# Optimization experiments

Measured on AMD Instinct MI355X. Metric: run time of the kernel, lower is better.

## Reference

```python
import jax, jax.numpy as jnp
import numpy as np

BETA = 0.25

def setup_inputs() -> dict:
    key = jax.random.key(0)
    k1, k2 = jax.random.split(key)
    z_e = jax.random.normal(k1, (32, 256, 32, 32), dtype=jnp.float32)
    embed_weight = jax.random.normal(k2, (4096, 256), dtype=jnp.float32) * 0.1
    return {"z_e": z_e, "embed_weight": embed_weight}

def reference(z_e, embed_weight):
    # Eval-mode forward (no input noise, no EMA buffer update).
    B, C, H, W = z_e.shape
    K = embed_weight.shape[0]
    z_t = jnp.transpose(z_e, (0, 2, 3, 1))            # [B,H,W,C]
    z_flat = z_t.reshape(-1, C)                        # [N,C]
    # Squared Euclidean distances; argmin is identical to argmin of cdist(p=2).
    d = (
        jnp.sum(z_flat * z_flat, axis=1, keepdims=True)
        - 2.0 * (z_flat @ embed_weight.T)
        + jnp.sum(embed_weight * embed_weight, axis=1)
    )                                                  # [N,K]
    idx = jnp.argmin(d, axis=1)                        # [N]
    # utilization = (#unique codes used) / vocab_size, jit-safe via bincount-style scatter
    counts = jnp.zeros((K,), dtype=jnp.float32).at[idx].add(1.0)
    utilization = jnp.sum(counts > 0).astype(jnp.float32) / K
    z_q = embed_weight[idx].reshape(B, H, W, C)        # [B,H,W,C]
    commitment_loss = jnp.mean((jax.lax.stop_gradient(z_q) - z_t) ** 2) * BETA
    z_q_st = z_t + jax.lax.stop_gradient(z_q - z_t)    # straight-through
    return jnp.transpose(z_q_st, (0, 3, 1, 2)), commitment_loss, utilization
```

## Files before the change

### kernel.cpp

```cpp
#include <hip/hip_runtime.h>
#include <math.h>


#define WGAP 52

using half8 = __attribute__((ext_vector_type(8))) _Float16;
using f32x4 = __attribute__((ext_vector_type(4))) float;

__device__ __forceinline__ void gload_lds16(const void* g, void* l) {
  __builtin_amdgcn_global_load_lds(
      (const __attribute__((address_space(1))) unsigned int*)g,
      (__attribute__((address_space(3))) unsigned int*)l, 16, 0, 0);
}

__device__ __forceinline__ bool lexlt64(double v, int x, double ov, int ox) {
  return (v < ov) || (v == ov && x < ox);
}

__device__ __forceinline__ int med3i(int a, int b, int c) {
  int d;
  asm("v_med3_i32 %0, %1, %2, %3" : "=v"(d) : "v"(a), "v"(b), "v"(c));
  return d;
}

__device__ __forceinline__ void ins3k(int key, int& a0, int& a1, int& a2) {
  const int n2 = min(a2, max(key, a1));
  const int n1 = med3i(key, a0, a1);
  a0 = min(key, a0);
  a1 = n1;
  a2 = n2;
}

__device__ __forceinline__ void mrg3k(int& a0, int& a1, int& a2,
                                      int b0, int b1, int b2) {
  const int c0 = min(a0, b0);
  const int x = max(a0, b0);
  const int y = min(a1, b1);
  const int c1 = min(x, y);
  const int z = max(x, y);
  const int ww = min(a2, b2);
  const int c2 = min(z, ww);
  a0 = c0; a1 = c1; a2 = c2;
}

__global__ __launch_bounds__(256) void vq_prep(const float* __restrict__ E,
                                               uint4* __restrict__ Epk,
                                               float* __restrict__ en1024,
                                               int* __restrict__ used,
                                               double* __restrict__ lossSum,
                                               int* __restrict__ candCount,
                                               int* __restrict__ messyCount) {
  const int t = blockIdx.x * 256 + threadIdx.x;
  if (t < 4096) used[t] = 0;
  if (t == 4096) *lossSum = 0.0;
  if (t == 4097) *candCount = 0;
  if (t == 4098) *messyCount = 0;
  const int code = t >> 5, j = t & 31;
  const int rc = code & 63;
  const int khalf = j >> 4, jo = j & 15;
  const float* src = E + (size_t)code * 256 + j * 8;
  const float4 v0 = *(const float4*)(src);
  const float4 v1 = *(const float4*)(src + 4);
  float zv[8] = {v0.x, v0.y, v0.z, v0.w, v1.x, v1.y, v1.z, v1.w};
  union { half8 h; uint4 u; } pk;
  float s = 0.f;
#pragma unroll
  for (int e = 0; e < 8; ++e) {
    const float z = zv[e];
    s = fmaf(z, z, s);
    pk.h[e] = (_Float16)(z * 256.0f);
  }
  const size_t g = (size_t)((code >> 6) * 2 + khalf) * 1024 +
                   rc * 16 + (jo ^ (rc & 15));
  Epk[g] = pk.u;
#pragma unroll
  for (int off = 1; off < 32; off <<= 1) s += __shfl_xor(s, off);
  if (j == 0) en1024[code] = s * 1024.0f;
}

__global__ __launch_bounds__(256, 3) void vq_screen(
    const float* __restrict__ Z, const char* __restrict__ Epk,
    const float* __restrict__ en1024,
    int* __restrict__ pk0, int* __restrict__ pk1, int* __restrict__ pk2) {
  __shared__ char lds[32768];
  const int tid = threadIdx.x;
  const int w = tid >> 6, l = tid & 63;
  const int xcd = blockIdx.x & 7, inner = blockIdx.x >> 3;
  const int part = inner % 3;
  const int qg = (inner / 3) * 8 + xcd;
  const int chs = part * 21 + (part > 0 ? 1 : 0);
  const int che = chs + (part == 0 ? 22 : 21);
  const int qbase = qg * 128;
  const int b = qbase >> 10;
  const int hwq = (qbase & 1023) + w * 32 + (l & 15);

  const float* Zq = Z + (size_t)b * 262144 + hwq;
  half8 ah[2][8];
#pragma unroll
  for (int u = 0; u < 2; ++u)
#pragma unroll
    for (int ks = 0; ks < 8; ++ks) {
      const int c0 = ks * 32 + (l >> 4) * 8;
#pragma unroll
      for (int e = 0; e < 8; ++e)
        ah[u][ks][e] = (_Float16)(Zq[u * 16 + ((size_t)(c0 + e) << 10)] * 256.0f);
    }

  int lo[4];
#pragma unroll
  for (int s = 0; s < 4; ++s)
    lo[s] = (l & 15) * 256 + (((s * 4 + (l >> 4)) ^ (l & 15)) << 4);

  int k0[2][4], k1[2][4], k2[2][4];
#pragma unroll
  for (int u = 0; u < 2; ++u)
#pragma unroll
    for (int r = 0; r < 4; ++r) {
      k0[u][r] = 0x7fffffff; k1[u][r] = 0x7fffffff; k2[u][r] = 0x7fffffff;
    }

  auto stage = [&](int sel, int ss) {
    const char* src = Epk + ((size_t)ss << 14) + w * 4096 + l * 16;
    char* dst = lds + sel * 16384 + w * 4096;
#pragma unroll
    for (int i = 0; i < 4; ++i) gload_lds16(src + i * 1024, dst + i * 1024);
  };
  stage(0, chs * 2);

  for (int ch = chs; ch < che; ++ch) {
    f32x4 acc[2][4];
#pragma unroll
    for (int u = 0; u < 2; ++u)
#pragma unroll
      for (int t = 0; t < 4; ++t) acc[u][t] = (f32x4){0.f, 0.f, 0.f, 0.f};

#pragma unroll
    for (int sh = 0; sh < 2; ++sh) {
      const int ss = ch * 2 + sh;
      __syncthreads();
      if (ss + 1 < che * 2) stage((ss + 1) & 1, ss + 1);
      const char* Lb = lds + (ss & 1) * 16384;
      __builtin_amdgcn_s_setprio(1);
#pragma unroll
      for (int s = 0; s < 4; ++s) {
        const int ks = sh * 4 + s;
#pragma unroll
        for (int t = 0; t < 4; ++t) {
          const half8 eh = *(const half8*)(Lb + t * 4096 + lo[s]);
          acc[0][t] = __builtin_amdgcn_mfma_f32_16x16x32_f16(ah[0][ks], eh, acc[0][t], 0, 0, 0);
          acc[1][t] = __builtin_amdgcn_mfma_f32_16x16x32_f16(ah[1][ks], eh, acc[1][t], 0, 0, 0);
        }
      }
      __builtin_amdgcn_s_setprio(0);
    }

    const int cb = ch * 64;
#pragma unroll
    for (int t = 0; t < 4; ++t) {
      const int code = cb + t * 16 + (l & 15);
      const float en = en1024[code];
#pragma unroll
      for (int u = 0; u < 2; ++u)
#pragma unroll
        for (int r = 0; r < 4; ++r) {
          const float df = fmaf(acc[u][t][r], -0.03125f, en);
          const int di = (int)df;
          const int key = (int)(((unsigned)di << 12) + (unsigned)code);
          ins3k(key, k0[u][r], k1[u][r], k2[u][r]);
        }
    }
  }

#pragma unroll
  for (int mask = 1; mask <= 8; mask <<= 1) {
#pragma unroll
    for (int u = 0; u < 2; ++u)
#pragma unroll
      for (int r = 0; r < 4; ++r) {
        const int o0 = __shfl_xor(k0[u][r], mask);
        const int o1 = __shfl_xor(k1[u][r], mask);
        const int o2 = __shfl_xor(k2[u][r], mask);
        mrg3k(k0[u][r], k1[u][r], k2[u][r], o0, o1, o2);
      }
  }
  if ((l & 15) == 0) {
#pragma unroll
    for (int u = 0; u < 2; ++u)
#pragma unroll
      for (int r = 0; r < 4; ++r) {
        const int n = qbase + w * 32 + u * 16 + (l >> 4) * 4 + r;
        const int o = part * 32768 + n;
        pk0[o] = k0[u][r]; pk1[o] = k1[u][r]; pk2[o] = k2[u][r];
      }
  }
}

__global__ __launch_bounds__(256) void vq_merge(
    const int* __restrict__ pk0, const int* __restrict__ pk1,
    const int* __restrict__ pk2, int* __restrict__ idxOut,
    int* __restrict__ cand, int* __restrict__ candCount,
    int* __restrict__ messy, int* __restrict__ messyCount,
    int* __restrict__ pi0, int* __restrict__ pi1, int* __restrict__ pi2) {
  const int n = blockIdx.x * 256 + threadIdx.x;
  int a0 = pk0[n], a1 = pk1[n], a2 = pk2[n];
#pragma unroll
  for (int q = 1; q < 3; ++q) {
    const int o = q * 32768 + n;
    mrg3k(a0, a1, a2, pk0[o], pk1[o], pk2[o]);
  }
  const int x0 = a0 & 0xfff;
  idxOut[n] = x0;
  const int d0 = a0 >> 12, d1 = a1 >> 12, d2 = a2 >> 12;
  if (d1 - d0 < WGAP) {
    if (d2 - d0 < WGAP) {
      const int p = atomicAdd(messyCount, 1);
      if (p < 4096) messy[p] = n;
    } else {
      const int p = atomicAdd(candCount, 1);
      cand[p] = n;
      pi0[n] = x0; pi1[n] = a1 & 0xfff; pi2[n] = a2 & 0xfff;
    }
  }
}

__global__ __launch_bounds__(256) void vq_exact(
    const float* __restrict__ Z, const float* __restrict__ E,
    const int* __restrict__ pi0, const int* __restrict__ pi1,
    const int* __restrict__ pi2, const int* __restrict__ cand,
    const int* __restrict__ candCount, const int* __restrict__ messy,
    const int* __restrict__ messyCount, double* __restrict__ parv,
    int* __restrict__ parx, int* __restrict__ idxOut) {
  __shared__ float zs[4][256];
  __shared__ double rv[4][256];
  __shared__ int ri[4][256];
  const int t = threadIdx.x;
  const int w = t >> 6, l = t & 63;

  if (blockIdx.x < 256) {
    const int cnt = *candCount;
    for (int j = blockIdx.x * 4 + w; j < cnt; j += 1024) {
      const int n = cand[j];
      const int b = n >> 10, hw = n & 1023;
      const int ca = pi0[n], cbn = pi1[n], cc = pi2[n];
      float z4[4];
#pragma unroll
      for (int i = 0; i < 4; ++i)
        z4[i] = Z[(size_t)b * 262144 + ((size_t)(l * 4 + i) << 10) + hw];
      const float4 e0 = *(const float4*)(E + (size_t)ca * 256 + l * 4);
      const float4 e1 = *(const float4*)(E + (size_t)cbn * 256 + l * 4);
      const float4 e2 = *(const float4*)(E + (size_t)cc * 256 + l * 4);
      double d0 = 0, d1 = 0, d2 = 0;
      const float* p0 = (const float*)&e0;
      const float* p1 = (const float*)&e1;
      const float* p2 = (const float*)&e2;
#pragma unroll
      for (int i = 0; i < 4; ++i) {
        const double f0 = (double)z4[i] - (double)p0[i];
        const double f1 = (double)z4[i] - (double)p1[i];
        const double f2 = (double)z4[i] - (double)p2[i];
        d0 = fma(f0, f0, d0);
        d1 = fma(f1, f1, d1);
        d2 = fma(f2, f2, d2);
      }
#pragma unroll
      for (int off = 32; off > 0; off >>= 1) {
        d0 += __shfl_down(d0, off);
        d1 += __shfl_down(d1, off);
        d2 += __shfl_down(d2, off);
      }
      if (l == 0) {
        double bv = d0; int bx = ca;
        if (lexlt64(d1, cbn, bv, bx)) { bv = d1; bx = cbn; }
        if (lexlt64(d2, cc, bv, bx)) { bv = d2; bx = cc; }
        idxOut[n] = bx;
      }
    }
    return;
  }

  const int cnt0 = *messyCount;
  const int cnt = cnt0 > 4096 ? 4096 : cnt0;
  const int jobs = ((cnt + 3) >> 2) * 16;
  for (int job = blockIdx.x - 256; job < jobs; job += 512) {
    const int grp = job >> 4, chunk = job & 15;
    __syncthreads();
    {
      const int q = t >> 6, lq = t & 63;
      const int mi = grp * 4 + q;
      const int n = messy[mi < cnt ? mi : grp * 4];
      const int b = n >> 10, hw = n & 1023;
#pragma unroll
      for (int i = 0; i < 4; ++i)
        zs[q][lq * 4 + i] =
            Z[(size_t)b * 262144 + ((size_t)(lq * 4 + i) << 10) + hw];
    }
    __syncthreads();
    const int code = chunk * 256 + t;
    const float* er = E + (size_t)code * 256;
    double s0 = 0, s1 = 0, s2 = 0, s3 = 0;
    for (int c = 0; c < 256; ++c) {
      const double ec = (double)er[c];
      const double f0 = (double)zs[0][c] - ec;
      const double f1 = (double)zs[1][c] - ec;
      const double f2 = (double)zs[2][c] - ec;
      const double f3 = (double)zs[3][c] - ec;
      s0 = fma(f0, f0, s0);
      s1 = fma(f1, f1, s1);
      s2 = fma(f2, f2, s2);
      s3 = fma(f3, f3, s3);
    }
    rv[0][t] = s0; rv[1][t] = s1; rv[2][t] = s2; rv[3][t] = s3;
    ri[0][t] = code; ri[1][t] = code; ri[2][t] = code; ri[3][t] = code;
    __syncthreads();
    for (int s = 128; s > 0; s >>= 1) {
      if (t < s) {
#pragma unroll
        for (int qq = 0; qq < 4; ++qq)
          if (lexlt64(rv[qq][t + s], ri[qq][t + s], rv[qq][t], ri[qq][t])) {
            rv[qq][t] = rv[qq][t + s];
            ri[qq][t] = ri[qq][t + s];
          }
      }
      __syncthreads();
    }
    if (t == 0) {
#pragma unroll
      for (int qq = 0; qq < 4; ++qq) {
        const int mi = grp * 4 + qq;
        if (mi < cnt) {
          parv[mi * 16 + chunk] = rv[qq][0];
          parx[mi * 16 + chunk] = ri[qq][0];
        }
      }
    }
  }
}

__global__ __launch_bounds__(256) void vq_messy2(
    const int* __restrict__ messy, const int* __restrict__ messyCount,
    const double* __restrict__ parv, const int* __restrict__ parx,
    int* __restrict__ idxOut) {
  const int cnt0 = *messyCount;
  const int cnt = cnt0 > 4096 ? 4096 : cnt0;
  for (int j = blockIdx.x * 256 + threadIdx.x; j < cnt; j += gridDim.x * 256) {
    double bv = parv[j * 16];
    int bx = parx[j * 16];
    for (int ch = 1; ch < 16; ++ch) {
      const double v = parv[j * 16 + ch];
      const int x = parx[j * 16 + ch];
      if (lexlt64(v, x, bv, bx)) { bv = v; bx = x; }
    }
    idxOut[messy[j]] = bx;
  }
}

__global__ __launch_bounds__(256) void vq_out(
    const float* __restrict__ Z, const float* __restrict__ E,
    const int* __restrict__ idx, float* __restrict__ out,
    double* __restrict__ lossSum, int* __restrict__ used) {
  __shared__ float zt[32][257];
  __shared__ int ids[32];
  const int tid = threadIdx.x;
  const int qb = blockIdx.x * 32;
  const int b = qb >> 10, hw0 = qb & 1023;
  if (tid < 32) {
    const int id = idx[qb + tid];
    ids[tid] = id;
    used[id] = 1;
  }
  __syncthreads();
  const int w = tid >> 6, l = tid & 63;
#pragma unroll
  for (int rr = 0; rr < 8; ++rr) {
    const int q = rr * 4 + w;
    const float4 v = *(const float4*)(E + (size_t)ids[q] * 256 + l * 4);
    zt[q][l * 4 + 0] = v.x;
    zt[q][l * 4 + 1] = v.y;
    zt[q][l * 4 + 2] = v.z;
    zt[q][l * 4 + 3] = v.w;
  }
  __syncthreads();
  const int h4 = (tid & 7) * 4;
  const int c0 = tid >> 3;
  float ls = 0.f;
#pragma unroll
  for (int p = 0; p < 8; ++p) {
    const int c = p * 32 + c0;
    const size_t g = (size_t)b * 262144 + ((size_t)c << 10) + hw0 + h4;
    const float4 z4 = *(const float4*)(Z + g);
    float4 o;
    o.x = zt[h4 + 0][c];
    o.y = zt[h4 + 1][c];
    o.z = zt[h4 + 2][c];
    o.w = zt[h4 + 3][c];
    *(float4*)(out + g) = o;
    const float dx = o.x - z4.x, dy = o.y - z4.y;
    const float dz = o.z - z4.z, dw = o.w - z4.w;
    ls = fmaf(dx, dx, ls);
    ls = fmaf(dy, dy, ls);
    ls = fmaf(dz, dz, ls);
    ls = fmaf(dw, dw, ls);
  }
#pragma unroll
  for (int off = 32; off > 0; off >>= 1) ls += __shfl_down(ls, off);
  __shared__ float red[4];
  if (l == 0) red[w] = ls;
  __syncthreads();
  if (tid == 0)
    atomicAdd(lossSum, (double)((red[0] + red[1]) + (red[2] + red[3])));
}

__global__ __launch_bounds__(256) void vq_final(const int* __restrict__ used,
                                                const double* __restrict__ lossSum,
                                                float* __restrict__ out) {
  __shared__ int cnt[256];
  int c = 0;
  for (int k = threadIdx.x; k < 4096; k += 256) c += (used[k] > 0);
  cnt[threadIdx.x] = c;
  __syncthreads();
  if (threadIdx.x == 0) {
    int tot = 0;
    for (int t = 0; t < 256; ++t) tot += cnt[t];
    out[8388608] = (float)(*lossSum * 0.25 / 8388608.0);
    out[8388609] = (float)tot / 4096.0f;
  }
}

extern "C" void kernel_launch(void* const* d_in, const int* in_sizes, int n_in,
                              void* d_out, int out_size, void* d_ws, size_t ws_size,
                              hipStream_t stream) {
  const float* Z = (const float*)d_in[0];
  const float* E = (const float*)d_in[1];
  float* out = (float*)d_out;
  char* w = (char*)d_ws;

  int* idx = (int*)w;
  int* cand = (int*)(w + 131072);
  float* en1024 = (float*)(w + 262144);
  int* used = (int*)(w + 278528);
  double* lossSum = (double*)(w + 294912);
  int* candCount = (int*)(w + 294920);
  int* messyCount = (int*)(w + 294924);

  char* Epk16 = (char*)out;
  int* pk0 = (int*)(out + 524288);
  int* pk1 = (int*)(out + 655360);
  int* pk2 = (int*)(out + 786432);
  int* pi0 = (int*)(out + 917504);
  int* pi1 = (int*)(out + 950272);
  int* pi2 = (int*)(out + 983040);
  int* messy = (int*)(out + 1015808);
  double* parv = (double*)(out + 1019904);
  int* parx = (int*)(out + 1150976);

  vq_prep<<<512, 256, 0, stream>>>(E, (uint4*)Epk16, en1024, used, lossSum,
                                   candCount, messyCount);
  vq_screen<<<768, 256, 0, stream>>>(Z, Epk16, en1024, pk0, pk1, pk2);
  vq_merge<<<128, 256, 0, stream>>>(pk0, pk1, pk2, idx, cand, candCount,
                                    messy, messyCount, pi0, pi1, pi2);
  vq_exact<<<768, 256, 0, stream>>>(Z, E, pi0, pi1, pi2, cand, candCount,
                                    messy, messyCount, parv, parx, idx);
  vq_messy2<<<8, 256, 0, stream>>>(messy, messyCount, parv, parx, idx);
  vq_out<<<1024, 256, 0, stream>>>(Z, E, idx, out, lossSum, used);
  vq_final<<<1, 256, 0, stream>>>(used, lossSum, out);
}
```

Baseline: 161.9 us.

## Use per-wave triple-buffered codebook staging without block barriers and fold distance bias into MFMA

Each wave now stages its own codebook slices into a private triple-buffered LDS region, synchronising with vmcnt waits instead of block-wide __syncthreads. The codebook is repacked into per-k-step 4KB tiles, and the sign and scaling are folded in so the accumulator starts at the code-norm term. This removes the per-chunk FMA before key construction. The aim is to remove barrier stalls and overlap loads with MFMA, at the cost of more LDS (48KB), which may reduce occupancy, and redundant loads of the same codebook data by every wave.

```diff
diff --git a/kernel.cpp b/kernel.cpp
--- a/kernel.cpp
+++ b/kernel.cpp
@@ -57,7 +57,6 @@
   if (t == 4098) *messyCount = 0;
   const int code = t >> 5, j = t & 31;
   const int rc = code & 63;
-  const int khalf = j >> 4, jo = j & 15;
   const float* src = E + (size_t)code * 256 + j * 8;
   const float4 v0 = *(const float4*)(src);
   const float4 v1 = *(const float4*)(src + 4);
@@ -68,10 +67,10 @@
   for (int e = 0; e < 8; ++e) {
     const float z = zv[e];
     s = fmaf(z, z, s);
-    pk.h[e] = (_Float16)(z * 256.0f);
-  }
-  const size_t g = (size_t)((code >> 6) * 2 + khalf) * 1024 +
-                   rc * 16 + (jo ^ (rc & 15));
+    pk.h[e] = (_Float16)(z * -256.0f);
+  }
+  const size_t g = (size_t)((code >> 6) * 8 + (j >> 2)) * 256 +
+                   rc * 4 + ((j & 3) ^ (rc & 3));
   Epk[g] = pk.u;
 #pragma unroll
   for (int off = 1; off < 32; off <<= 1) s += __shfl_xor(s, off);
@@ -82,7 +81,7 @@
     const float* __restrict__ Z, const char* __restrict__ Epk,
     const float* __restrict__ en1024,
     int* __restrict__ pk0, int* __restrict__ pk1, int* __restrict__ pk2) {
-  __shared__ char lds[32768];
+  __shared__ char lds[49152];
   const int tid = threadIdx.x;
   const int w = tid >> 6, l = tid & 63;
   const int xcd = blockIdx.x & 7, inner = blockIdx.x >> 3;
@@ -90,10 +89,23 @@
   const int qg = (inner / 3) * 8 + xcd;
   const int chs = part * 21 + (part > 0 ? 1 : 0);
   const int che = chs + (part == 0 ? 22 : 21);
+  const int S = (che - chs) * 8;
   const int qbase = qg * 128;
   const int b = qbase >> 10;
   const int hwq = (qbase & 1023) + w * 32 + (l & 15);
 
+  char* myLds = lds + w * 12288;
+  const char* EpkBase = Epk + ((size_t)(chs * 8) << 12) + l * 16;
+
+  auto stage = [&](int q, int slot) {
+    const char* src = EpkBase + ((size_t)q << 12);
+    char* dst = myLds + slot * 4096;
+#pragma unroll
+    for (int i = 0; i < 4; ++i) gload_lds16(src + i * 1024, dst + i * 1024);
+  };
+  stage(0, 0);
+  stage(1, 1);
+
   const float* Zq = Z + (size_t)b * 262144 + hwq;
   half8 ah[2][8];
 #pragma unroll
@@ -103,13 +115,10 @@
       const int c0 = ks * 32 + (l >> 4) * 8;
 #pragma unroll
       for (int e = 0; e < 8; ++e)
-        ah[u][ks][e] = (_Float16)(Zq[u * 16 + ((size_t)(c0 + e) << 10)] * 256.0f);
-    }
-
-  int lo[4];
-#pragma unroll
-  for (int s = 0; s < 4; ++s)
-    lo[s] = (l & 15) * 256 + (((s * 4 + (l >> 4)) ^ (l & 15)) << 4);
+        ah[u][ks][e] = (_Float16)(Zq[u * 16 + ((size_t)(c0 + e) << 10)] * 8.0f);
+    }
+
+  const int lo0 = (l & 15) * 64 + (((l >> 4) ^ (l & 3)) << 4);
 
   int k0[2][4], k1[2][4], k2[2][4];
 #pragma unroll
@@ -119,52 +128,47 @@
       k0[u][r] = 0x7fffffff; k1[u][r] = 0x7fffffff; k2[u][r] = 0x7fffffff;
     }
 
-  auto stage = [&](int sel, int ss) {
-    const char* src = Epk + ((size_t)ss << 14) + w * 4096 + l * 16;
-    char* dst = lds + sel * 16384 + w * 4096;
-#pragma unroll
-    for (int i = 0; i < 4; ++i) gload_lds16(src + i * 1024, dst + i * 1024);
-  };
-  stage(0, chs * 2);
-
+  int cur = 0, pf = 2, q = 0;
   for (int ch = chs; ch < che; ++ch) {
+    const int cb = ch * 64;
     f32x4 acc[2][4];
 #pragma unroll
-    for (int u = 0; u < 2; ++u)
-#pragma unroll
-      for (int t = 0; t < 4; ++t) acc[u][t] = (f32x4){0.f, 0.f, 0.f, 0.f};
-
-#pragma unroll
-    for (int sh = 0; sh < 2; ++sh) {
-      const int ss = ch * 2 + sh;
-      __syncthreads();
-      if (ss + 1 < che * 2) stage((ss + 1) & 1, ss + 1);
-      const char* Lb = lds + (ss & 1) * 16384;
+    for (int t = 0; t < 4; ++t) {
+      const float en = en1024[cb + t * 16 + (l & 15)];
+      acc[0][t] = (f32x4){en, en, en, en};
+      acc[1][t] = (f32x4){en, en, en, en};
+    }
+
+#pragma unroll
+    for (int ks = 0; ks < 8; ++ks) {
+      if (q + 2 < S) {
+        stage(q + 2, pf);
+        asm volatile("s_waitcnt vmcnt(8)" ::: "memory");
+      } else {
+        asm volatile("s_waitcnt vmcnt(0)" ::: "memory");
+      }
+      const char* Lb = myLds + cur * 4096;
       __builtin_amdgcn_s_setprio(1);
 #pragma unroll
-      for (int s = 0; s < 4; ++s) {
-        const int ks = sh * 4 + s;
-#pragma unroll
-        for (int t = 0; t < 4; ++t) {
-          const half8 eh = *(const half8*)(Lb + t * 4096 + lo[s]);
-          acc[0][t] = __builtin_amdgcn_mfma_f32_16x16x32_f16(ah[0][ks], eh, acc[0][t], 0, 0, 0);
-          acc[1][t] = __builtin_amdgcn_mfma_f32_16x16x32_f16(ah[1][ks], eh, acc[1][t], 0, 0, 0);
-        }
+      for (int t = 0; t < 4; ++t) {
+        const half8 eh = *(const half8*)(Lb + lo0 + t * 1024);
+        acc[0][t] = __builtin_amdgcn_mfma_f32_16x16x32_f16(ah[0][ks], eh, acc[0][t], 0, 0, 0);
+        acc[1][t] = __builtin_amdgcn_mfma_f32_16x16x32_f16(ah[1][ks], eh, acc[1][t], 0, 0, 0);
       }
       __builtin_amdgcn_s_setprio(0);
-    }
-
-    const int cb = ch * 64;
+      cur = (cur == 2) ? 0 : cur + 1;
+      pf = (pf == 2) ? 0 : pf + 1;
+      ++q;
+    }
+
 #pragma unroll
     for (int t = 0; t < 4; ++t) {
       const int code = cb + t * 16 + (l & 15);
-      const float en = en1024[code];
 #pragma unroll
       for (int u = 0; u < 2; ++u)
 #pragma unroll
         for (int r = 0; r < 4; ++r) {
-          const float df = fmaf(acc[u][t][r], -0.03125f, en);
-          const int di = (int)df;
+          const int di = (int)acc[u][t][r];
           const int key = (int)(((unsigned)di << 12) + (unsigned)code);
           ins3k(key, k0[u][r], k1[u][r], k2[u][r]);
         }
```

Result: slower. 182.6 us (+12.8%).
